# Performance work log

Measured on AMD Instinct MI355X. Metric: run time of the kernel, lower is better.

Reference implementation:

```python
import jax, jax.numpy as jnp
import numpy as np

N_HEAD = 16

def setup_inputs() -> dict:
    key = jax.random.key(0)
    k1, k2, k3 = jax.random.split(key, 3)
    B, S, D = 2, 2048, 1024
    std = 0.02
    return {
        "hidden_states": jax.random.normal(k1, (B, S, D), jnp.float32),
        "w_attn": jax.random.normal(k2, (D, 3 * D), jnp.float32) * std,
        "b_attn": jnp.zeros((3 * D,), jnp.float32),
        "w_proj": jax.random.normal(k3, (D, D), jnp.float32) * std,
        "b_proj": jnp.zeros((D,), jnp.float32),
    }

def reference(hidden_states, w_attn, b_attn, w_proj, b_proj):
    B, S, D = hidden_states.shape
    H = N_HEAD
    hd = D // H
    # fused qkv projection (Conv1D == x @ W + b)
    qkv = hidden_states @ w_attn + b_attn            # [B,S,3D]
    q, k, v = jnp.split(qkv, 3, axis=-1)
    def split_heads(t):
        return t.reshape(B, S, H, hd).transpose(0, 2, 1, 3)  # [B,H,S,hd]
    q, k, v = split_heads(q), split_heads(k), split_heads(v)
    # scores with scale = sqrt(head_dim)
    scores = jnp.einsum('bhqd,bhkd->bhqk', q, k) / jnp.sqrt(jnp.asarray(hd, q.dtype))
    causal = jnp.tril(jnp.ones((S, S), bool))
    mask_value = jnp.finfo(scores.dtype).min
    scores = jnp.where(causal, scores, mask_value)
    attn = jax.nn.softmax(scores, axis=-1)           # dropout p=0 (eval)
    out = jnp.einsum('bhqk,bhkd->bhqd', attn, v)     # [B,H,S,hd]
    out = out.transpose(0, 2, 1, 3).reshape(B, S, D)
    out = out @ w_proj + b_proj
    return out
```

## Files before the change

kernel.cpp:

```cpp
#include <hip/hip_runtime.h>

#define S_LEN 2048
#define D_MODEL 1024
#define NHEAD 16
#define HDIM 64
#define BATCH 2
#define M_ROWS (BATCH * S_LEN)
#define N_QKV (3 * D_MODEL)
#define QSCALE 0.18033688011112042f

typedef __attribute__((ext_vector_type(8))) short bf16x8;
typedef __attribute__((ext_vector_type(4))) float f32x4;

static __device__ __forceinline__ unsigned short f2bf(float f) {
  unsigned int u = __float_as_uint(f);
  u += 0x7FFFu + ((u >> 16) & 1u);
  return (unsigned short)(u >> 16);
}
static __device__ __forceinline__ unsigned int pkbf(float a, float b) {
  unsigned int ua = __float_as_uint(a) + 0x8000u;
  unsigned int ub = __float_as_uint(b) + 0x8000u;
  return __builtin_amdgcn_perm(ub, ua, 0x07060302u);
}

static __device__ __forceinline__ void async_cp16(unsigned short* lds, const unsigned short* g) {
  __builtin_amdgcn_global_load_lds((__attribute__((address_space(1))) void*)g,
                                   (__attribute__((address_space(3))) void*)lds, 16, 0, 0);
}

__global__ __launch_bounds__(256) void k_prep(const float* __restrict__ x,
                                              unsigned short* __restrict__ xb,
                                              const float* __restrict__ w_attn,
                                              unsigned short* __restrict__ wqkvT,
                                              const float* __restrict__ w_proj,
                                              unsigned short* __restrict__ wprojT) {
  __shared__ unsigned short T[32][33];
  const int blk = blockIdx.x;
  const int tid = threadIdx.x;
  if (blk < 4096) {
    int i = blk * 256 + tid;
    float4 v = ((const float4*)x)[i];
    ushort4 o;
    o.x = f2bf(v.x); o.y = f2bf(v.y); o.z = f2bf(v.z); o.w = f2bf(v.w);
    ((ushort4*)xb)[i] = o;
    return;
  }
  const float* w;
  unsigned short* wT;
  int bid, Ndim;
  if (blk < 7168) { bid = blk - 4096; w = w_attn; wT = wqkvT; Ndim = N_QKV; }
  else            { bid = blk - 7168; w = w_proj; wT = wprojT; Ndim = D_MODEL; }
  const int nb = Ndim / 32;
  const int n0 = (bid % nb) * 32, k0 = (bid / nb) * 32;
  const int tx = tid & 31, ty = tid >> 5;
#pragma unroll
  for (int j = 0; j < 4; ++j) {
    int r = ty + j * 8;
    T[r][tx] = f2bf(w[(size_t)(k0 + r) * Ndim + n0 + tx]);
  }
  __syncthreads();
#pragma unroll
  for (int j = 0; j < 4; ++j) {
    int r = ty + j * 8;
    wT[(size_t)(n0 + r) * D_MODEL + k0 + tx] = T[tx][r];
  }
}

__global__ __launch_bounds__(256) void k_gemm_qkv(const unsigned short* __restrict__ A,
                                                  const unsigned short* __restrict__ Bt,
                                                  const float* __restrict__ bias,
                                                  unsigned short* __restrict__ Qb,
                                                  unsigned short* __restrict__ Kbuf,
                                                  unsigned short* __restrict__ VTb) {
  __shared__ __align__(16) unsigned short As[2][128 * 32];
  __shared__ __align__(16) unsigned short Bs[2][128 * 32];
  const int tid = threadIdx.x;
  const int wid = tid >> 6, lane = tid & 63;
  const int lr = lane & 15, lg = lane >> 4;
  const int blk = blockIdx.x;
  const int xcd = blk & 7, idx = blk >> 3;
  const int bm = ((xcd & 3) * 8 + (idx & 7)) * 128;
  const int bn = ((xcd >> 2) * 12 + (idx >> 3)) * 128;
  const int wm = (wid >> 1) * 64, wn = (wid & 1) * 64;
  const int K = D_MODEL;
  const int c0 = tid, c1 = tid + 256;
  const size_t a0o = (size_t)(bm + (c0 >> 2)) * K + (c0 & 3) * 8;
  const size_t a1o = (size_t)(bm + (c1 >> 2)) * K + (c1 & 3) * 8;
  const size_t b0o = (size_t)(bn + (c0 >> 2)) * K + (c0 & 3) * 8;
  const size_t b1o = (size_t)(bn + (c1 >> 2)) * K + (c1 & 3) * 8;

  f32x4 acc[4][4] = {};

  async_cp16(&As[0][c0 * 8], &A[a0o]);
  async_cp16(&As[0][c1 * 8], &A[a1o]);
  async_cp16(&Bs[0][c0 * 8], &Bt[b0o]);
  async_cp16(&Bs[0][c1 * 8], &Bt[b1o]);

  for (int k0 = 0; k0 < K; k0 += 32) {
    const int p = (k0 >> 5) & 1;
    __syncthreads();
    if (k0 + 32 < K) {
      async_cp16(&As[p ^ 1][c0 * 8], &A[a0o + k0 + 32]);
      async_cp16(&As[p ^ 1][c1 * 8], &A[a1o + k0 + 32]);
      async_cp16(&Bs[p ^ 1][c0 * 8], &Bt[b0o + k0 + 32]);
      async_cp16(&Bs[p ^ 1][c1 * 8], &Bt[b1o + k0 + 32]);
    }
    bf16x8 af[4], bfr[4];
#pragma unroll
    for (int i = 0; i < 4; ++i) af[i] = *(const bf16x8*)&As[p][(wm + i * 16 + lr) * 32 + lg * 8];
#pragma unroll
    for (int t = 0; t < 4; ++t) bfr[t] = *(const bf16x8*)&Bs[p][(wn + t * 16 + lr) * 32 + lg * 8];
#pragma unroll
    for (int i = 0; i < 4; ++i)
#pragma unroll
      for (int t = 0; t < 4; ++t)
        acc[i][t] = __builtin_amdgcn_mfma_f32_16x16x32_bf16(af[i], bfr[t], acc[i][t], 0, 0, 0);
  }
#pragma unroll
  for (int i = 0; i < 4; ++i) {
#pragma unroll
    for (int t = 0; t < 4; ++t) {
      int n = bn + wn + t * 16 + lr;
      int part = n >> 10, rem = n & 1023;
      int h = rem >> 6, d = rem & 63;
      float bv = bias[n];
      int row0 = bm + wm + i * 16 + lg * 4;
      int bb = row0 >> 11, s0 = row0 & 2047;
      if (part == 2) {
        ushort4 vv;
        vv.x = f2bf(acc[i][t][0] + bv);
        vv.y = f2bf(acc[i][t][1] + bv);
        vv.z = f2bf(acc[i][t][2] + bv);
        vv.w = f2bf(acc[i][t][3] + bv);
        *(ushort4*)&VTb[(((size_t)(bb << 4) + h) * HDIM + d) * S_LEN + s0] = vv;
      } else {
        unsigned short* dst = (part == 0) ? Qb : Kbuf;
        float sc = (part == 0) ? QSCALE : 1.0f;
#pragma unroll
        for (int r = 0; r < 4; ++r)
          dst[(((size_t)(bb << 4) + h) * S_LEN + (s0 + r)) * HDIM + d] = f2bf((acc[i][t][r] + bv) * sc);
      }
    }
  }
}

__global__ __launch_bounds__(256) void k_gemm_proj(const unsigned short* __restrict__ A,
                                                   const unsigned short* __restrict__ Bt,
                                                   const float* __restrict__ bias,
                                                   float* __restrict__ out) {
  __shared__ __align__(16) unsigned short As[2][128 * 32];
  __shared__ __align__(16) unsigned short Bs[2][128 * 32];
  const int tid = threadIdx.x;
  const int wid = tid >> 6, lane = tid & 63;
  const int lr = lane & 15, lg = lane >> 4;
  const int blk = blockIdx.x;
  const int xcd = blk & 7, idx = blk >> 3;
  const int bm = (xcd * 4 + (idx & 3)) * 128;
  const int bn = (idx >> 2) * 128;
  const int wm = (wid >> 1) * 64, wn = (wid & 1) * 64;
  const int K = D_MODEL;
  const int c0 = tid, c1 = tid + 256;
  const size_t a0o = (size_t)(bm + (c0 >> 2)) * K + (c0 & 3) * 8;
  const size_t a1o = (size_t)(bm + (c1 >> 2)) * K + (c1 & 3) * 8;
  const size_t b0o = (size_t)(bn + (c0 >> 2)) * K + (c0 & 3) * 8;
  const size_t b1o = (size_t)(bn + (c1 >> 2)) * K + (c1 & 3) * 8;

  f32x4 acc[4][4] = {};

  async_cp16(&As[0][c0 * 8], &A[a0o]);
  async_cp16(&As[0][c1 * 8], &A[a1o]);
  async_cp16(&Bs[0][c0 * 8], &Bt[b0o]);
  async_cp16(&Bs[0][c1 * 8], &Bt[b1o]);

  for (int k0 = 0; k0 < K; k0 += 32) {
    const int p = (k0 >> 5) & 1;
    __syncthreads();
    if (k0 + 32 < K) {
      async_cp16(&As[p ^ 1][c0 * 8], &A[a0o + k0 + 32]);
      async_cp16(&As[p ^ 1][c1 * 8], &A[a1o + k0 + 32]);
      async_cp16(&Bs[p ^ 1][c0 * 8], &Bt[b0o + k0 + 32]);
      async_cp16(&Bs[p ^ 1][c1 * 8], &Bt[b1o + k0 + 32]);
    }
    bf16x8 af[4], bfr[4];
#pragma unroll
    for (int i = 0; i < 4; ++i) af[i] = *(const bf16x8*)&As[p][(wm + i * 16 + lr) * 32 + lg * 8];
#pragma unroll
    for (int t = 0; t < 4; ++t) bfr[t] = *(const bf16x8*)&Bs[p][(wn + t * 16 + lr) * 32 + lg * 8];
#pragma unroll
    for (int i = 0; i < 4; ++i)
#pragma unroll
      for (int t = 0; t < 4; ++t)
        acc[i][t] = __builtin_amdgcn_mfma_f32_16x16x32_bf16(af[i], bfr[t], acc[i][t], 0, 0, 0);
  }
#pragma unroll
  for (int i = 0; i < 4; ++i) {
#pragma unroll
    for (int t = 0; t < 4; ++t) {
      int n = bn + wn + t * 16 + lr;
      float bv = bias[n];
#pragma unroll
      for (int r = 0; r < 4; ++r) {
        int row = bm + wm + i * 16 + lg * 4 + r;
        out[(size_t)row * D_MODEL + n] = acc[i][t][r] + bv;
      }
    }
  }
}

__global__ __launch_bounds__(256, 2) void k_attn7(const unsigned short* __restrict__ Qb,
                                                  const unsigned short* __restrict__ Kb,
                                                  const unsigned short* __restrict__ VT,
                                                  unsigned short* __restrict__ AO) {
  const int tid = threadIdx.x;
  const int wid = tid >> 6, lane = tid & 63;
  const int lr = lane & 15, quad = lane >> 4;
  const int blk = blockIdx.x;
  const int bh = blk & 31;
  const int g = blk >> 5;
  const int slot = (g < 8) ? g : 23 - g;
  const int b = bh >> 4, h = bh & 15;

  __shared__ __align__(16) unsigned short Ks[2][64 * 64];
  __shared__ __align__(16) unsigned short Vs[2][64 * 64];
  __shared__ __align__(16) unsigned short Pbuf[4][16 * 72];
  unsigned short* pb = &Pbuf[wid][0];

  const unsigned short* Kbh = Kb + (size_t)bh * S_LEN * HDIM;
  const unsigned short* VTbh = VT + (size_t)bh * HDIM * S_LEN;

  const int sL = slot * 4 + wid;
  const int Rs[2] = {sL * 16, (127 - sL) * 16};
  const int ntile = ((127 - slot * 4) >> 2) + 1;

  bf16x8 qf[2][2];
#pragma unroll
  for (int st = 0; st < 2; ++st)
#pragma unroll
    for (int dh = 0; dh < 2; ++dh)
      qf[st][dh] = *(const bf16x8*)&Qb[((size_t)bh * S_LEN + Rs[st] + lr) * HDIM + dh * 32 + quad * 8];

  f32x4 Ot[2][4] = {};
  float ms[2] = {-1e30f, -1e30f};
  float ls[2] = {0.f, 0.f};

  const int srow = lane >> 3;
  const int scol = ((lane & 7) ^ srow) * 8;

#pragma unroll
  for (int j = 0; j < 2; ++j) {
    const int r0 = wid * 16 + j * 8;
    async_cp16(&Ks[0][r0 * 64 + lane * 8], &Kbh[(size_t)(r0 + srow) * HDIM + scol]);
    async_cp16(&Vs[0][r0 * 64 + lane * 8], &VTbh[(size_t)(r0 + srow) * S_LEN + scol]);
  }

  for (int kt = 0; kt < ntile; ++kt) {
    const int k0 = kt * 64;
    const int p = kt & 1;
    __syncthreads();
    if (kt + 1 < ntile) {
      const int kn = k0 + 64;
#pragma unroll
      for (int j = 0; j < 2; ++j) {
        const int r0 = wid * 16 + j * 8;
        async_cp16(&Ks[p ^ 1][r0 * 64 + lane * 8], &Kbh[(size_t)(kn + r0 + srow) * HDIM + scol]);
        async_cp16(&Vs[p ^ 1][r0 * 64 + lane * 8], &VTbh[(size_t)(r0 + srow) * S_LEN + kn + scol]);
      }
    }

    bf16x8 kf[4][2], vf[4][2];
#pragma unroll
    for (int kg = 0; kg < 4; ++kg)
#pragma unroll
      for (int dh = 0; dh < 2; ++dh)
        kf[kg][dh] = *(const bf16x8*)&Ks[p][(kg * 16 + lr) * 64 + (((dh * 4 + quad) ^ (lr & 7)) * 8)];
#pragma unroll
    for (int dg = 0; dg < 4; ++dg)
#pragma unroll
      for (int kh = 0; kh < 2; ++kh)
        vf[dg][kh] = *(const bf16x8*)&Vs[p][(dg * 16 + lr) * 64 + (((kh * 4 + quad) ^ (lr & 7)) * 8)];

#pragma unroll
    for (int st = 0; st < 2; ++st) {
      const int R = Rs[st];
      if (k0 > R + 15) continue;
      f32x4 Sv[4];
#pragma unroll
      for (int kg = 0; kg < 4; ++kg) {
        f32x4 a = {};
        a = __builtin_amdgcn_mfma_f32_16x16x32_bf16(kf[kg][0], qf[st][0], a, 0, 0, 0);
        a = __builtin_amdgcn_mfma_f32_16x16x32_bf16(kf[kg][1], qf[st][1], a, 0, 0, 0);
        Sv[kg] = a;
      }
      if (k0 + 63 > R) {
        const int q = R + lr;
#pragma unroll
        for (int kg = 0; kg < 4; ++kg)
#pragma unroll
          for (int r = 0; r < 4; ++r)
            if (k0 + kg * 16 + quad * 4 + r > q) Sv[kg][r] = -1e30f;
      }
      float mx = ms[st];
#pragma unroll
      for (int kg = 0; kg < 4; ++kg)
        mx = fmaxf(mx, fmaxf(fmaxf(Sv[kg][0], Sv[kg][1]), fmaxf(Sv[kg][2], Sv[kg][3])));
      mx = fmaxf(mx, __shfl_xor(mx, 16));
      mx = fmaxf(mx, __shfl_xor(mx, 32));
      const float alpha = __builtin_amdgcn_exp2f(ms[st] - mx);
      ms[st] = mx;
      float rs = 0.f;
#pragma unroll
      for (int kg = 0; kg < 4; ++kg) {
        float e0 = __builtin_amdgcn_exp2f(Sv[kg][0] - mx);
        float e1 = __builtin_amdgcn_exp2f(Sv[kg][1] - mx);
        float e2 = __builtin_amdgcn_exp2f(Sv[kg][2] - mx);
        float e3 = __builtin_amdgcn_exp2f(Sv[kg][3] - mx);
        rs += (e0 + e1) + (e2 + e3);
        *(unsigned int*)&pb[lr * 72 + kg * 16 + quad * 4]     = pkbf(e0, e1);
        *(unsigned int*)&pb[lr * 72 + kg * 16 + quad * 4 + 2] = pkbf(e2, e3);
      }
      rs += __shfl_xor(rs, 16);
      rs += __shfl_xor(rs, 32);
      ls[st] = ls[st] * alpha + rs;
#pragma unroll
      for (int dg = 0; dg < 4; ++dg)
#pragma unroll
        for (int r = 0; r < 4; ++r) Ot[st][dg][r] *= alpha;
      bf16x8 pf0 = *(const bf16x8*)&pb[lr * 72 + quad * 8];
      bf16x8 pf1 = *(const bf16x8*)&pb[lr * 72 + 32 + quad * 8];
#pragma unroll
      for (int dg = 0; dg < 4; ++dg) {
        Ot[st][dg] = __builtin_amdgcn_mfma_f32_16x16x32_bf16(vf[dg][0], pf0, Ot[st][dg], 0, 0, 0);
        Ot[st][dg] = __builtin_amdgcn_mfma_f32_16x16x32_bf16(vf[dg][1], pf1, Ot[st][dg], 0, 0, 0);
      }
    }
  }

#pragma unroll
  for (int st = 0; st < 2; ++st) {
    const float rl = __builtin_amdgcn_rcpf(ls[st]);
    const int s = Rs[st] + lr;
#pragma unroll
    for (int dg = 0; dg < 4; ++dg) {
      const size_t o = ((size_t)b * S_LEN + s) * D_MODEL + h * 64 + dg * 16 + quad * 4;
      *(unsigned int*)&AO[o]     = pkbf(Ot[st][dg][0] * rl, Ot[st][dg][1] * rl);
      *(unsigned int*)&AO[o + 2] = pkbf(Ot[st][dg][2] * rl, Ot[st][dg][3] * rl);
    }
  }
}

extern "C" void kernel_launch(void* const* d_in, const int* in_sizes, int n_in,
                              void* d_out, int out_size, void* d_ws, size_t ws_size,
                              hipStream_t stream) {
  const float* x      = (const float*)d_in[0];
  const float* w_attn = (const float*)d_in[1];
  const float* b_attn = (const float*)d_in[2];
  const float* w_proj = (const float*)d_in[3];
  const float* b_proj = (const float*)d_in[4];
  float* out = (float*)d_out;

  unsigned short* ws     = (unsigned short*)d_ws;
  unsigned short* xb     = ws;
  unsigned short* wqkvT  = xb + (size_t)M_ROWS * D_MODEL;
  unsigned short* wprojT = wqkvT + (size_t)N_QKV * D_MODEL;
  unsigned short* Qb     = wprojT + (size_t)D_MODEL * D_MODEL;
  unsigned short* Kb     = Qb + (size_t)M_ROWS * D_MODEL;
  unsigned short* VT     = Kb + (size_t)M_ROWS * D_MODEL;
  unsigned short* AO     = xb;

  k_prep<<<8192, 256, 0, stream>>>(x, xb, w_attn, wqkvT, w_proj, wprojT);
  k_gemm_qkv<<<768, 256, 0, stream>>>(xb, wqkvT, b_attn, Qb, Kb, VT);
  k_attn7<<<512, 256, 0, stream>>>(Qb, Kb, VT, AO);
  k_gemm_proj<<<256, 256, 0, stream>>>(AO, wprojT, b_proj, out);
}
```

Before: 179.9 us.

## Keep softmax probabilities in registers via 16x16x16 MFMA and split query-strip pairing

```diff
diff --git a/kernel.cpp b/kernel.cpp
--- a/kernel.cpp
+++ b/kernel.cpp
@@ -10,7 +10,18 @@
 #define QSCALE 0.18033688011112042f
 
 typedef __attribute__((ext_vector_type(8))) short bf16x8;
+typedef __attribute__((ext_vector_type(4))) short bf16x4;
 typedef __attribute__((ext_vector_type(4))) float f32x4;
+
+#if __has_builtin(__builtin_amdgcn_mfma_f32_16x16x16bf16_1k)
+#define MFMA1616(A, B, C) __builtin_amdgcn_mfma_f32_16x16x16bf16_1k((A), (B), (C), 0, 0, 0)
+#else
+static __device__ __forceinline__ f32x4 mfma1616_asm(bf16x4 a, bf16x4 b, f32x4 c) {
+  asm("v_mfma_f32_16x16x16_bf16 %0, %1, %2, %0" : "+v"(c) : "v"(a), "v"(b));
+  return c;
+}
+#define MFMA1616(A, B, C) mfma1616_asm((A), (B), (C))
+#endif
 
 static __device__ __forceinline__ unsigned short f2bf(float f) {
   unsigned int u = __float_as_uint(f);
@@ -207,7 +218,7 @@
   }
 }
 
-__global__ __launch_bounds__(256, 2) void k_attn7(const unsigned short* __restrict__ Qb,
+__global__ __launch_bounds__(256, 4) void k_attn8(const unsigned short* __restrict__ Qb,
                                                   const unsigned short* __restrict__ Kb,
                                                   const unsigned short* __restrict__ VT,
                                                   unsigned short* __restrict__ AO) {
@@ -217,31 +228,25 @@
   const int blk = blockIdx.x;
   const int bh = blk & 31;
   const int g = blk >> 5;
-  const int slot = (g < 8) ? g : 23 - g;
   const int b = bh >> 4, h = bh & 15;
+  const int sL = (g < 16) ? (g * 4 + wid) : (127 - ((g - 16) * 4 + wid));
+  const int R = sL * 16;
+  const int ntile = (sL >> 2) + 1;
 
   __shared__ __align__(16) unsigned short Ks[2][64 * 64];
   __shared__ __align__(16) unsigned short Vs[2][64 * 64];
-  __shared__ __align__(16) unsigned short Pbuf[4][16 * 72];
-  unsigned short* pb = &Pbuf[wid][0];
 
   const unsigned short* Kbh = Kb + (size_t)bh * S_LEN * HDIM;
   const unsigned short* VTbh = VT + (size_t)bh * HDIM * S_LEN;
 
-  const int sL = slot * 4 + wid;
-  const int Rs[2] = {sL * 16, (127 - sL) * 16};
-  const int ntile = ((127 - slot * 4) >> 2) + 1;
-
-  bf16x8 qf[2][2];
-#pragma unroll
-  for (int st = 0; st < 2; ++st)
-#pragma unroll
-    for (int dh = 0; dh < 2; ++dh)
-      qf[st][dh] = *(const bf16x8*)&Qb[((size_t)bh * S_LEN + Rs[st] + lr) * HDIM + dh * 32 + quad * 8];
-
-  f32x4 Ot[2][4] = {};
-  float ms[2] = {-1e30f, -1e30f};
-  float ls[2] = {0.f, 0.f};
+  bf16x8 qf[2];
+#pragma unroll
+  for (int dh = 0; dh < 2; ++dh)
+    qf[dh] = *(const bf16x8*)&Qb[((size_t)bh * S_LEN + R + lr) * HDIM + dh * 32 + quad * 8];
+
+  f32x4 Ot[4] = {};
+  float ms = -1e30f;
+  float ls = 0.f;
 
   const int srow = lane >> 3;
   const int scol = ((lane & 7) ^ srow) * 8;
@@ -267,84 +272,79 @@
       }
     }
 
-    bf16x8 kf[4][2], vf[4][2];
+    bf16x8 kf[4][2];
 #pragma unroll
     for (int kg = 0; kg < 4; ++kg)
 #pragma unroll
       for (int dh = 0; dh < 2; ++dh)
         kf[kg][dh] = *(const bf16x8*)&Ks[p][(kg * 16 + lr) * 64 + (((dh * 4 + quad) ^ (lr & 7)) * 8)];
+
+    f32x4 Sv[4];
+#pragma unroll
+    for (int kg = 0; kg < 4; ++kg) {
+      f32x4 a = {};
+      a = __builtin_amdgcn_mfma_f32_16x16x32_bf16(kf[kg][0], qf[0], a, 0, 0, 0);
+      a = __builtin_amdgcn_mfma_f32_16x16x32_bf16(kf[kg][1], qf[1], a, 0, 0, 0);
+      Sv[kg] = a;
+    }
+    if (k0 + 63 > R) {
+      const int q = R + lr;
+#pragma unroll
+      for (int kg = 0; kg < 4; ++kg)
+#pragma unroll
+        for (int r = 0; r < 4; ++r)
+          if (k0 + kg * 16 + quad * 4 + r > q) Sv[kg][r] = -1e30f;
+    }
+    float mx = ms;
+#pragma unroll
+    for (int kg = 0; kg < 4; ++kg)
+      mx = fmaxf(mx, fmaxf(fmaxf(Sv[kg][0], Sv[kg][1]), fmaxf(Sv[kg][2], Sv[kg][3])));
+    mx = fmaxf(mx, __shfl_xor(mx, 16));
+    mx = fmaxf(mx, __shfl_xor(mx, 32));
+    const float alpha = __builtin_amdgcn_exp2f(ms - mx);
+    ms = mx;
+    bf16x4 pf[4];
+    float rs = 0.f;
+#pragma unroll
+    for (int kg = 0; kg < 4; ++kg) {
+      float e0 = __builtin_amdgcn_exp2f(Sv[kg][0] - mx);
+      float e1 = __builtin_amdgcn_exp2f(Sv[kg][1] - mx);
+      float e2 = __builtin_amdgcn_exp2f(Sv[kg][2] - mx);
+      float e3 = __builtin_amdgcn_exp2f(Sv[kg][3] - mx);
+      rs += (e0 + e1) + (e2 + e3);
+      union { bf16x4 v; unsigned int u[2]; } pu;
+      pu.u[0] = pkbf(e0, e1);
+      pu.u[1] = pkbf(e2, e3);
+      pf[kg] = pu.v;
+    }
+    rs += __shfl_xor(rs, 16);
+    rs += __shfl_xor(rs, 32);
+    ls = ls * alpha + rs;
 #pragma unroll
     for (int dg = 0; dg < 4; ++dg)
 #pragma unroll
-      for (int kh = 0; kh < 2; ++kh)
-        vf[dg][kh] = *(const bf16x8*)&Vs[p][(dg * 16 + lr) * 64 + (((kh * 4 + quad) ^ (lr & 7)) * 8)];
-
-#pragma unroll
-    for (int st = 0; st < 2; ++st) {
-      const int R = Rs[st];
-      if (k0 > R + 15) continue;
-      f32x4 Sv[4];
-#pragma unroll
-      for (int kg = 0; kg < 4; ++kg) {
-        f32x4 a = {};
-        a = __builtin_amdgcn_mfma_f32_16x16x32_bf16(kf[kg][0], qf[st][0], a, 0, 0, 0);
-        a = __builtin_amdgcn_mfma_f32_16x16x32_bf16(kf[kg][1], qf[st][1], a, 0, 0, 0);
-        Sv[kg] = a;
-      }
-      if (k0 + 63 > R) {
-        const int q = R + lr;
-#pragma unroll
-        for (int kg = 0; kg < 4; ++kg)
-#pragma unroll
-          for (int r = 0; r < 4; ++r)
-            if (k0 + kg * 16 + quad * 4 + r > q) Sv[kg][r] = -1e30f;
-      }
-      float mx = ms[st];
+      for (int r = 0; r < 4; ++r) Ot[dg][r] *= alpha;
+
+#pragma unroll
+    for (int dg = 0; dg < 4; ++dg) {
+      bf16x4 vf[4];
 #pragma unroll
       for (int kg = 0; kg < 4; ++kg)
-        mx = fmaxf(mx, fmaxf(fmaxf(Sv[kg][0], Sv[kg][1]), fmaxf(Sv[kg][2], Sv[kg][3])));
-      mx = fmaxf(mx, __shfl_xor(mx, 16));
-      mx = fmaxf(mx, __shfl_xor(mx, 32));
-      const float alpha = __builtin_amdgcn_exp2f(ms[st] - mx);
-      ms[st] = mx;
-      float rs = 0.f;
-#pragma unroll
-      for (int kg = 0; kg < 4; ++kg) {
-        float e0 = __builtin_amdgcn_exp2f(Sv[kg][0] - mx);
-        float e1 = __builtin_amdgcn_exp2f(Sv[kg][1] - mx);
-        float e2 = __builtin_amdgcn_exp2f(Sv[kg][2] - mx);
-        float e3 = __builtin_amdgcn_exp2f(Sv[kg][3] - mx);
-        rs += (e0 + e1) + (e2 + e3);
-        *(unsigned int*)&pb[lr * 72 + kg * 16 + quad * 4]     = pkbf(e0, e1);
-        *(unsigned int*)&pb[lr * 72 + kg * 16 + quad * 4 + 2] = pkbf(e2, e3);
-      }
-      rs += __shfl_xor(rs, 16);
-      rs += __shfl_xor(rs, 32);
-      ls[st] = ls[st] * alpha + rs;
-#pragma unroll
-      for (int dg = 0; dg < 4; ++dg)
-#pragma unroll
-        for (int r = 0; r < 4; ++r) Ot[st][dg][r] *= alpha;
-      bf16x8 pf0 = *(const bf16x8*)&pb[lr * 72 + quad * 8];
-      bf16x8 pf1 = *(const bf16x8*)&pb[lr * 72 + 32 + quad * 8];
-#pragma unroll
-      for (int dg = 0; dg < 4; ++dg) {
-        Ot[st][dg] = __builtin_amdgcn_mfma_f32_16x16x32_bf16(vf[dg][0], pf0, Ot[st][dg], 0, 0, 0);
-        Ot[st][dg] = __builtin_amdgcn_mfma_f32_16x16x32_bf16(vf[dg][1], pf1, Ot[st][dg], 0, 0, 0);
-      }
-    }
-  }
-
-#pragma unroll
-  for (int st = 0; st < 2; ++st) {
-    const float rl = __builtin_amdgcn_rcpf(ls[st]);
-    const int s = Rs[st] + lr;
-#pragma unroll
-    for (int dg = 0; dg < 4; ++dg) {
-      const size_t o = ((size_t)b * S_LEN + s) * D_MODEL + h * 64 + dg * 16 + quad * 4;
-      *(unsigned int*)&AO[o]     = pkbf(Ot[st][dg][0] * rl, Ot[st][dg][1] * rl);
-      *(unsigned int*)&AO[o + 2] = pkbf(Ot[st][dg][2] * rl, Ot[st][dg][3] * rl);
-    }
+        vf[kg] = *(const bf16x4*)&Vs[p][(dg * 16 + lr) * 64 +
+                                        (((kg * 2 + (quad >> 1)) ^ (lr & 7)) * 8) + (quad & 1) * 4];
+#pragma unroll
+      for (int kg = 0; kg < 4; ++kg)
+        Ot[dg] = MFMA1616(vf[kg], pf[kg], Ot[dg]);
+    }
+  }
+
+  const float rl = __builtin_amdgcn_rcpf(ls);
+  const int s = R + lr;
+#pragma unroll
+  for (int dg = 0; dg < 4; ++dg) {
+    const size_t o = ((size_t)b * S_LEN + s) * D_MODEL + h * 64 + dg * 16 + quad * 4;
+    *(unsigned int*)&AO[o]     = pkbf(Ot[dg][0] * rl, Ot[dg][1] * rl);
+    *(unsigned int*)&AO[o + 2] = pkbf(Ot[dg][2] * rl, Ot[dg][3] * rl);
   }
 }
 
@@ -369,6 +369,6 @@
 
   k_prep<<<8192, 256, 0, stream>>>(x, xb, w_attn, wqkvT, w_proj, wprojT);
   k_gemm_qkv<<<768, 256, 0, stream>>>(xb, wqkvT, b_attn, Qb, Kb, VT);
-  k_attn7<<<512, 256, 0, stream>>>(Qb, Kb, VT, AO);
+  k_attn8<<<1024, 256, 0, stream>>>(Qb, Kb, VT, AO);
   k_gemm_proj<<<256, 256, 0, stream>>>(AO, wprojT, b_proj, out);
 }
```

Measured after the change: 181.6 us. Within noise of the previous version (+0.9%).
